# Optimization experiments

Measured on AMD Instinct MI355X. Metric: run time of the kernel, lower is better.

## Reference

```python
import jax, jax.numpy as jnp
import numpy as np

# dims (match init_kwargs / input_specs)
B, T, D = 64, 512, 128
H = 256          # hidden_size
W = 32           # cell_size
N = 64           # n_slots
R = 4            # n_reads
L = 2            # ctl_n_layers
TAU = 0.3
CLIP = 20.0
RW = R * W                      # read_size = 128
CTL_IN = D + RW                 # 256
CTL_OUT = 2 * RW + W + W        # 2*read + write cell + erase = 320
EPS = 1e-8


def setup_inputs() -> dict:
    key = jax.random.key(0)
    ks = jax.random.split(key, 10)
    s = lambda k, shape: jax.random.normal(k, shape, jnp.float32) * 0.05
    return {
        "x": jax.random.normal(ks[0], (B, T, D), jnp.float32),
        "h0": jax.random.normal(ks[1], (L, B, H), jnp.float32) * 0.1,
        # GRU layer 0 (PyTorch layout: [3H, in])
        "W_ih0": s(ks[2], (3 * H, CTL_IN)), "W_hh0": s(ks[3], (3 * H, H)),
        "b_ih0": jnp.zeros((3 * H,), jnp.float32), "b_hh0": jnp.zeros((3 * H,), jnp.float32),
        # GRU layer 1
        "W_ih1": s(ks[4], (3 * H, H)), "W_hh1": s(ks[5], (3 * H, H)),
        "b_ih1": jnp.zeros((3 * H,), jnp.float32), "b_hh1": jnp.zeros((3 * H,), jnp.float32),
        # interface Linear(H -> CTL_OUT) + ReLU
        "W_int": s(ks[6], (CTL_OUT, H)), "b_int": jnp.zeros((CTL_OUT,), jnp.float32),
        # mix gate Linear(2W -> W)
        "W_mix": s(ks[7], (W, 2 * W)), "b_mix": jnp.zeros((W,), jnp.float32),
    }


def _gru(xt, h, Wih, Whh, bih, bhh):
    gi = xt @ Wih.T + bih
    gh = h @ Whh.T + bhh
    ir, iz, inn = jnp.split(gi, 3, axis=-1)
    hr, hz, hn = jnp.split(gh, 3, axis=-1)
    r = jax.nn.sigmoid(ir + hr)
    z = jax.nn.sigmoid(iz + hz)
    n = jnp.tanh(inn + r * hn)
    return (1.0 - z) * n + z * h


def _cos_read(k, M, tau):
    # k: [b,R,W] keys, M: [b,N,W] memory -> content-based softmax read
    kn = k / (jnp.linalg.norm(k, axis=-1, keepdims=True) + EPS)
    Mn = M / (jnp.linalg.norm(M, axis=-1, keepdims=True) + EPS)
    w = jax.nn.softmax(jnp.einsum('brw,bnw->brn', kn, Mn) / tau, axis=-1)
    return jnp.einsum('brn,bnw->brw', w, M), w


def _forward(x, h0, W_ih0, W_hh0, b_ih0, b_hh0, W_ih1, W_hh1, b_ih1, b_hh1,
             W_int, b_int, W_mix, b_mix):
    bs = x.shape[0]

    def step(carry, inp):
        h0c, h1c, em, bm, l_read = carry
        xt, t = inp
        ctl = jnp.concatenate([xt, l_read], axis=-1)
        h0n = _gru(ctl, h0c, W_ih0, W_hh0, b_ih0, b_hh0)
        h1n = _gru(h0n, h1c, W_ih1, W_hh1, b_ih1, b_hh1)
        itf = jnp.clip(jax.nn.relu(h1n @ W_int.T + b_int), -CLIP, CLIP)
        k_em = itf[:, :RW].reshape(bs, R, W)
        k_bm = itf[:, RW:2 * RW].reshape(bs, R, W)
        m_t = itf[:, 2 * RW:2 * RW + W]          # write vector
        e_t = itf[:, 2 * RW + W:]                # erase vector
        # explicit memory: round-robin slot write (slot = t mod N), erase old content
        oh = jax.nn.one_hot(t % N, N, dtype=em.dtype)            # [N]
        em_erased = jnp.einsum('n,bnw->bw', oh, em)              # evicted slot
        em_new = em * (1.0 - oh)[None, :, None] + oh[None, :, None] * m_t[:, None, :]
        em_read, _ = _cos_read(k_em, em_new, TAU)
        # blurred memory: content read, then erase/accumulate evicted explicit slot
        bm_read, wb = _cos_read(k_bm, bm, 1.0)
        ww = wb.mean(axis=1)                                     # [b,N] write weights
        e = jax.nn.sigmoid(e_t)                                  # [b,W] bounded erase
        bm_new = bm * (1.0 - ww[:, :, None] * e[:, None, :]) \
                 + ww[:, :, None] * em_erased[:, None, :]
        # mix gate between explicit and blurred reads (per read head)
        g = jax.nn.sigmoid(jnp.concatenate([em_read, bm_read], -1) @ W_mix.T + b_mix)
        read = g * em_read + (1.0 - g) * bm_read                 # [b,R,W]
        l_new = read.reshape(bs, RW)
        out_t = jnp.concatenate([h0n, h1n, l_new], axis=-1)      # [b, 2H+RW]
        return (h0n, h1n, em_new, bm_new, l_new), out_t

    em0 = jnp.zeros((bs, N, W), x.dtype)
    bm0 = jnp.zeros((bs, N, W), x.dtype)
    lr0 = jnp.zeros((bs, RW), x.dtype)
    carry0 = (h0[0], h0[1], em0, bm0, lr0)
    xs = (jnp.swapaxes(x, 0, 1), jnp.arange(x.shape[1]))
    _, outs = jax.lax.scan(step, carry0, xs)                     # [T,b,2H+RW]
    return jnp.swapaxes(outs, 0, 1)                              # [b,T,2H+RW]


def reference(x, h0, W_ih0, W_hh0, b_ih0, b_hh0, W_ih1, W_hh1, b_ih1, b_hh1,
              W_int, b_int, W_mix, b_mix):
    return _forward(x, h0, W_ih0, W_hh0, b_ih0, b_hh0, W_ih1, W_hh1, b_ih1,
                    b_hh1, W_int, b_int, W_mix, b_mix)
```

## Files before the change

kernel.cpp:

```cpp
#include <hip/hip_runtime.h>
#include <hip/hip_bf16.h>
#include <stdint.h>

typedef unsigned int uint;
typedef unsigned short ushort;

#define TPB 768

#define OFF_A0 0
#define OFF_A1 (768*256)
#define OFF_A2 (2*768*256)
#define OFF_A3 (3*768*256)
#define OFF_A4 (4*768*256)
#define WS_USHORTS (4*768*256 + 320*256)

__device__ __forceinline__ float bflo(uint u){ return __uint_as_float(u << 16); }
__device__ __forceinline__ float bfhi(uint u){ return __uint_as_float(u & 0xffff0000u); }
__device__ __forceinline__ float sigm(float x){ return 1.0f / (1.0f + __expf(-x)); }
__device__ __forceinline__ float tanh_(float x){
    float xc = fminf(fmaxf(x, -15.0f), 15.0f);
    float e  = __expf(2.0f * xc);
    return (e - 1.0f) / (e + 1.0f);
}

__global__ void prep_kernel(const float* __restrict__ Wih0, const float* __restrict__ Whh0,
                            const float* __restrict__ Wih1, const float* __restrict__ Whh1,
                            const float* __restrict__ Wint, ushort* __restrict__ ws)
{
    int idx = blockIdx.x * 256 + threadIdx.x;
    if (idx >= WS_USHORTS) return;
    const float* src; int rows; int base; int p;
    if (idx < 4*768*256) {
        int m = idx / (768*256); p = idx % (768*256);
        src  = (m==0) ? Wih0 : (m==1) ? Whh0 : (m==2) ? Wih1 : Whh1;
        rows = 768; base = m * (768*256);
    } else {
        p = idx - 4*768*256; src = Wint; rows = 320; base = 4*768*256;
    }
    int kb  = p / (rows*8);
    int rem = p - kb*(rows*8);
    int j   = rem >> 3;
    int kl  = rem & 7;
    int k   = kb*8 + kl;
    __hip_bfloat16 h = __float2bfloat16(src[j*256 + k]);
    ws[base + p] = *reinterpret_cast<ushort*>(&h);
}

__device__ __forceinline__ void dual_mv(const ushort* __restrict__ Wi, const ushort* __restrict__ Wh,
                                        const float* vin, const float* hin,
                                        const float* __restrict__ bi, const float* __restrict__ bh,
                                        float* go_i, float* go_h, int tid)
{
    int j = tid;
    float ai = bi[j], ah = bh[j];
    const uint4* Pi = (const uint4*)Wi;
    const uint4* Ph = (const uint4*)Wh;
#pragma unroll 4
    for (int kb = 0; kb < 32; ++kb) {
        uint4 wi = Pi[kb*768 + j];
        uint4 wh = Ph[kb*768 + j];
        float4 va = *(const float4*)&vin[kb*8];
        float4 vb = *(const float4*)&vin[kb*8 + 4];
        float4 ha = *(const float4*)&hin[kb*8];
        float4 hb = *(const float4*)&hin[kb*8 + 4];
        ai += bflo(wi.x)*va.x + bfhi(wi.x)*va.y + bflo(wi.y)*va.z + bfhi(wi.y)*va.w
            + bflo(wi.z)*vb.x + bfhi(wi.z)*vb.y + bflo(wi.w)*vb.z + bfhi(wi.w)*vb.w;
        ah += bflo(wh.x)*ha.x + bfhi(wh.x)*ha.y + bflo(wh.y)*ha.z + bfhi(wh.y)*ha.w
            + bflo(wh.z)*hb.x + bfhi(wh.z)*hb.y + bflo(wh.w)*hb.z + bfhi(wh.w)*hb.w;
    }
    go_i[j] = ai; go_h[j] = ah;
}

__global__ __launch_bounds__(TPB) void ebm_main(
    const float* __restrict__ x, const float* __restrict__ h0i,
    const float* __restrict__ b_ih0, const float* __restrict__ b_hh0,
    const float* __restrict__ b_ih1, const float* __restrict__ b_hh1,
    const float* __restrict__ b_int, const float* __restrict__ Wmix,
    const float* __restrict__ bmix,
    const ushort* __restrict__ ws, float* __restrict__ out)
{
    __shared__ float v[256];
    __shared__ float gi[768], gh[768];
    __shared__ float h0s[256], h1s[256];
    __shared__ float lread[128];
    __shared__ float em[64][33], bm[64][33];
    __shared__ float itf[320];
    __shared__ float minv_em[64], minv_bm[64], kinv[8];
    __shared__ float sc[8][64];
    __shared__ float wwv[64], ev[32], emer[32];
    __shared__ float emrd[4][32], bmrd[4][32];
    __shared__ float wmix_s[32][65];

    const int tid = threadIdx.x;
    const int b   = blockIdx.x;

    if (tid < 256) { h0s[tid] = h0i[b*256 + tid]; h1s[tid] = h0i[(64 + b)*256 + tid]; }
    for (int i = tid; i < 64*33; i += TPB) { (&em[0][0])[i] = 0.f; (&bm[0][0])[i] = 0.f; }
    if (tid < 128) lread[tid] = 0.f;
    for (int i = tid; i < 32*64; i += TPB) { wmix_s[i >> 6][i & 63] = Wmix[i]; }
    __syncthreads();

    for (int t = 0; t < 512; ++t) {
        const size_t outbase = ((size_t)b*512 + t) * 640;

        if (tid < 128)      v[tid] = x[((size_t)b*512 + t)*128 + tid];
        else if (tid < 256) v[tid] = lread[tid - 128];
        __syncthreads();

        dual_mv(ws + OFF_A0, ws + OFF_A1, v, h0s, b_ih0, b_hh0, gi, gh, tid);
        __syncthreads();
        if (tid < 256) {
            float r  = sigm(gi[tid]       + gh[tid]);
            float z  = sigm(gi[256 + tid] + gh[256 + tid]);
            float n  = tanh_(gi[512 + tid] + r * gh[512 + tid]);
            float hn = (1.f - z) * n + z * h0s[tid];
            h0s[tid] = hn;
            out[outbase + tid] = hn;
        }
        __syncthreads();

        dual_mv(ws + OFF_A2, ws + OFF_A3, h0s, h1s, b_ih1, b_hh1, gi, gh, tid);
        __syncthreads();
        if (tid < 256) {
            float r  = sigm(gi[tid]       + gh[tid]);
            float z  = sigm(gi[256 + tid] + gh[256 + tid]);
            float n  = tanh_(gi[512 + tid] + r * gh[512 + tid]);
            float hn = (1.f - z) * n + z * h1s[tid];
            h1s[tid] = hn;
            out[outbase + 256 + tid] = hn;
        }
        __syncthreads();

        if (tid < 320) {
            float a = b_int[tid];
            const uint4* Pv = (const uint4*)(ws + OFF_A4);
#pragma unroll 4
            for (int kb = 0; kb < 32; ++kb) {
                uint4 wv = Pv[kb*320 + tid];
                float4 va = *(const float4*)&h1s[kb*8];
                float4 vb = *(const float4*)&h1s[kb*8 + 4];
                a += bflo(wv.x)*va.x + bfhi(wv.x)*va.y + bflo(wv.y)*va.z + bfhi(wv.y)*va.w
                   + bflo(wv.z)*vb.x + bfhi(wv.z)*vb.y + bflo(wv.w)*vb.z + bfhi(wv.w)*vb.w;
            }
            itf[tid] = fminf(fmaxf(a, 0.f), 20.f);
        }
        __syncthreads();

        const int slot = t & 63;
        if (tid < 32) {
            emer[tid] = em[slot][tid];
            em[slot][tid] = itf[256 + tid];
            ev[tid] = sigm(itf[288 + tid]);
        }
        if (tid >= 32 && tid < 40) {
            int r = tid - 32;
            const float* kk = &itf[r*32];
            float s = 0.f;
#pragma unroll
            for (int w2 = 0; w2 < 32; ++w2) { float q = kk[w2]; s += q*q; }
            kinv[r] = 1.f / (sqrtf(s) + 1e-8f);
        }
        __syncthreads();

        if (tid < 64) {
            float s = 0.f;
#pragma unroll
            for (int w2 = 0; w2 < 32; ++w2) { float q = em[tid][w2]; s += q*q; }
            minv_em[tid] = 1.f / (sqrtf(s) + 1e-8f);
        } else if (tid < 128) {
            int n = tid - 64; float s = 0.f;
#pragma unroll
            for (int w2 = 0; w2 < 32; ++w2) { float q = bm[n][w2]; s += q*q; }
            minv_bm[n] = 1.f / (sqrtf(s) + 1e-8f);
        }
        __syncthreads();

        if (tid < 512) {
            int mm = tid >> 8, r = (tid >> 6) & 3, n = tid & 63;
            const float* kk = &itf[mm*128 + r*32];
            const float (*M)[33] = mm ? bm : em;
            float d = 0.f;
#pragma unroll
            for (int w2 = 0; w2 < 32; ++w2) d += kk[w2] * M[n][w2];
            float val = d * kinv[mm*4 + r] * (mm ? minv_bm[n] : minv_em[n]);
            if (!mm) val /= 0.3f;
            sc[mm*4 + r][n] = val;
        }
        __syncthreads();

        {
            int wave = tid >> 6, lane = tid & 63;
            if (wave < 8) {
                float val = sc[wave][lane];
                float m = val;
                for (int o = 32; o > 0; o >>= 1) m = fmaxf(m, __shfl_xor(m, o));
                float e = __expf(val - m);
                float s = e;
                for (int o = 32; o > 0; o >>= 1) s += __shfl_xor(s, o);
                sc[wave][lane] = e / s;
            }
        }
        __syncthreads();

        if (tid < 64) wwv[tid] = 0.25f * (sc[4][tid] + sc[5][tid] + sc[6][tid] + sc[7][tid]);
        if (tid < 256) {
            int mm = tid >> 7, r = (tid >> 5) & 3, w2 = tid & 31;
            const float (*M)[33] = mm ? bm : em;
            const float* wr = sc[mm*4 + r];
            float a = 0.f;
#pragma unroll 8
            for (int n = 0; n < 64; ++n) a += wr[n] * M[n][w2];
            if (mm) bmrd[r][w2] = a; else emrd[r][w2] = a;
        }
        __syncthreads();

        if (tid < 128) {
            int r = tid >> 5, w2 = tid & 31;
            float a = bmix[w2];
#pragma unroll
            for (int c = 0; c < 32; ++c) a += wmix_s[w2][c]      * emrd[r][c];
#pragma unroll
            for (int c = 0; c < 32; ++c) a += wmix_s[w2][32 + c] * bmrd[r][c];
            float g  = sigm(a);
            float rd = g * emrd[r][w2] + (1.f - g) * bmrd[r][w2];
            lread[tid] = rd;
            out[outbase + 512 + tid] = rd;
        } else {
            for (int i2 = tid - 128; i2 < 2048; i2 += TPB - 128) {
                int n = i2 >> 5, w2 = i2 & 31;
                bm[n][w2] = bm[n][w2] * (1.f - wwv[n]*ev[w2]) + wwv[n]*emer[w2];
            }
        }
        __syncthreads();
    }
}

extern "C" void kernel_launch(void* const* d_in, const int* in_sizes, int n_in,
                              void* d_out, int out_size, void* d_ws, size_t ws_size,
                              hipStream_t stream)
{
    const float* x    = (const float*)d_in[0];
    const float* h0   = (const float*)d_in[1];
    const float* Wih0 = (const float*)d_in[2];
    const float* Whh0 = (const float*)d_in[3];
    const float* bih0 = (const float*)d_in[4];
    const float* bhh0 = (const float*)d_in[5];
    const float* Wih1 = (const float*)d_in[6];
    const float* Whh1 = (const float*)d_in[7];
    const float* bih1 = (const float*)d_in[8];
    const float* bhh1 = (const float*)d_in[9];
    const float* Wint = (const float*)d_in[10];
    const float* bint = (const float*)d_in[11];
    const float* Wmix = (const float*)d_in[12];
    const float* bmix = (const float*)d_in[13];
    ushort* ws = (ushort*)d_ws;
    float*  out = (float*)d_out;

    if (ws_size < (size_t)WS_USHORTS * sizeof(ushort)) return;

    prep_kernel<<<(WS_USHORTS + 255)/256, 256, 0, stream>>>(Wih0, Whh0, Wih1, Whh1, Wint, ws);
    ebm_main<<<64, TPB, 0, stream>>>(x, h0, bih0, bhh0, bih1, bhh1, bint, Wmix, bmix, ws, out);
}
```

Before: 12.03 ms.

## Split each batch's GRU across four cooperating blocks with global-flag syncs

Each batch row is now handled by four 256-thread blocks instead of one 768-thread block. Each block computes a quarter of the GRU gate rows and shares the new hidden states with the others through a global buffer, using release fences and spin-waits on per-step flags. The memory-read part is computed redundantly in all four blocks. The goal is to use more CUs and cut the per-block weight streaming on the serial recurrence, in exchange for two cross-block handshakes per timestep and repeated memory work. It also relies on all 256 blocks being resident at once, or the spin-waits deadlock.

```diff
diff --git a/kernel.cpp b/kernel.cpp
--- a/kernel.cpp
+++ b/kernel.cpp
@@ -5,7 +5,7 @@
 typedef unsigned int uint;
 typedef unsigned short ushort;
 
-#define TPB 768
+#define TPB 256
 
 #define OFF_A0 0
 #define OFF_A1 (768*256)
@@ -13,6 +13,9 @@
 #define OFF_A3 (3*768*256)
 #define OFF_A4 (4*768*256)
 #define WS_USHORTS (4*768*256 + 320*256)
+#define WB_BYTES ((size_t)WS_USHORTS * 2)
+#define HX_FLOATS (2*2*64*256)
+#define FL_UINTS (2*64*4)
 
 __device__ __forceinline__ float bflo(uint u){ return __uint_as_float(u << 16); }
 __device__ __forceinline__ float bfhi(uint u){ return __uint_as_float(u & 0xffff0000u); }
@@ -25,9 +28,11 @@
 
 __global__ void prep_kernel(const float* __restrict__ Wih0, const float* __restrict__ Whh0,
                             const float* __restrict__ Wih1, const float* __restrict__ Whh1,
-                            const float* __restrict__ Wint, ushort* __restrict__ ws)
+                            const float* __restrict__ Wint, ushort* __restrict__ ws,
+                            uint* __restrict__ fl)
 {
     int idx = blockIdx.x * 256 + threadIdx.x;
+    if (idx < FL_UINTS) fl[idx] = 0u;
     if (idx >= WS_USHORTS) return;
     const float* src; int rows; int base; int p;
     if (idx < 4*768*256) {
@@ -46,15 +51,30 @@
     ws[base + p] = *reinterpret_cast<ushort*>(&h);
 }
 
-__device__ __forceinline__ void dual_mv(const ushort* __restrict__ Wi, const ushort* __restrict__ Wh,
-                                        const float* vin, const float* hin,
-                                        const float* __restrict__ bi, const float* __restrict__ bh,
-                                        float* go_i, float* go_h, int tid)
-{
-    int j = tid;
-    float ai = bi[j], ah = bh[j];
+template<int ROWS>
+__device__ __forceinline__ float mv_row(const ushort* __restrict__ W, const float* vin,
+                                        float acc, int j)
+{
+    const uint4* P = (const uint4*)W;
+    float a0 = acc, a1 = 0.f;
+#pragma unroll 4
+    for (int kb = 0; kb < 32; ++kb) {
+        uint4 w = P[kb*ROWS + j];
+        float4 va = *(const float4*)&vin[kb*8];
+        float4 vb = *(const float4*)&vin[kb*8 + 4];
+        a0 += bflo(w.x)*va.x + bfhi(w.x)*va.y + bflo(w.y)*va.z + bfhi(w.y)*va.w;
+        a1 += bflo(w.z)*vb.x + bfhi(w.z)*vb.y + bflo(w.w)*vb.z + bfhi(w.w)*vb.w;
+    }
+    return a0 + a1;
+}
+
+__device__ __forceinline__ void dual_mv2(const ushort* __restrict__ Wi, const ushort* __restrict__ Wh,
+                                         const float* vin, const float* hin,
+                                         float bi, float bh, float* oi, float* oh, int j)
+{
     const uint4* Pi = (const uint4*)Wi;
     const uint4* Ph = (const uint4*)Wh;
+    float ai = bi, ah = bh;
 #pragma unroll 4
     for (int kb = 0; kb < 32; ++kb) {
         uint4 wi = Pi[kb*768 + j];
@@ -68,7 +88,17 @@
         ah += bflo(wh.x)*ha.x + bfhi(wh.x)*ha.y + bflo(wh.y)*ha.z + bfhi(wh.y)*ha.w
             + bflo(wh.z)*hb.x + bfhi(wh.z)*hb.y + bflo(wh.w)*hb.z + bfhi(wh.w)*hb.w;
     }
-    go_i[j] = ai; go_h[j] = ah;
+    *oi = ai; *oh = ah;
+}
+
+__device__ __forceinline__ void spin_ge(uint* f, uint v){
+    while (__hip_atomic_load(f, __ATOMIC_RELAXED, __HIP_MEMORY_SCOPE_AGENT) < v) {}
+}
+__device__ __forceinline__ float coh_ld(float* p){
+    return __hip_atomic_load(p, __ATOMIC_RELAXED, __HIP_MEMORY_SCOPE_AGENT);
+}
+__device__ __forceinline__ void coh_st(float* p, float v){
+    __hip_atomic_store(p, v, __ATOMIC_RELAXED, __HIP_MEMORY_SCOPE_AGENT);
 }
 
 __global__ __launch_bounds__(TPB) void ebm_main(
@@ -77,10 +107,11 @@
     const float* __restrict__ b_ih1, const float* __restrict__ b_hh1,
     const float* __restrict__ b_int, const float* __restrict__ Wmix,
     const float* __restrict__ bmix,
-    const ushort* __restrict__ ws, float* __restrict__ out)
+    const ushort* __restrict__ ws, float* __restrict__ hx, uint* __restrict__ fl,
+    float* __restrict__ out)
 {
     __shared__ float v[256];
-    __shared__ float gi[768], gh[768];
+    __shared__ float gi[192], gh[192];
     __shared__ float h0s[256], h1s[256];
     __shared__ float lread[128];
     __shared__ float em[64][33], bm[64][33];
@@ -92,57 +123,94 @@
     __shared__ float wmix_s[32][65];
 
     const int tid = threadIdx.x;
-    const int b   = blockIdx.x;
-
-    if (tid < 256) { h0s[tid] = h0i[b*256 + tid]; h1s[tid] = h0i[(64 + b)*256 + tid]; }
+    const int b   = blockIdx.x & 63;
+    const int q   = blockIdx.x >> 6;
+
+    h0s[tid] = h0i[b*256 + tid];
+    h1s[tid] = h0i[(64 + b)*256 + tid];
     for (int i = tid; i < 64*33; i += TPB) { (&em[0][0])[i] = 0.f; (&bm[0][0])[i] = 0.f; }
     if (tid < 128) lread[tid] = 0.f;
-    for (int i = tid; i < 32*64; i += TPB) { wmix_s[i >> 6][i & 63] = Wmix[i]; }
+    for (int i = tid; i < 32*64; i += TPB) wmix_s[i >> 6][i & 63] = Wmix[i];
     __syncthreads();
 
     for (int t = 0; t < 512; ++t) {
         const size_t outbase = ((size_t)b*512 + t) * 640;
-
-        if (tid < 128)      v[tid] = x[((size_t)b*512 + t)*128 + tid];
-        else if (tid < 256) v[tid] = lread[tid - 128];
-        __syncthreads();
-
-        dual_mv(ws + OFF_A0, ws + OFF_A1, v, h0s, b_ih0, b_hh0, gi, gh, tid);
-        __syncthreads();
-        if (tid < 256) {
+        const int par = t & 1;
+        const uint tv = (uint)(t + 1);
+
+        if (tid < 128) v[tid] = x[((size_t)b*512 + t)*128 + tid];
+        else           v[tid] = lread[tid - 128];
+        __syncthreads();
+
+        if (tid < 192) {
+            int g = tid >> 6, i = tid & 63;
+            int j = g*256 + q*64 + i;
+            dual_mv2(ws + OFF_A0, ws + OFF_A1, v, h0s, b_ih0[j], b_hh0[j], &gi[tid], &gh[tid], j);
+        }
+        __syncthreads();
+        if (tid < 64) {
             float r  = sigm(gi[tid]       + gh[tid]);
-            float z  = sigm(gi[256 + tid] + gh[256 + tid]);
-            float n  = tanh_(gi[512 + tid] + r * gh[512 + tid]);
-            float hn = (1.f - z) * n + z * h0s[tid];
-            h0s[tid] = hn;
-            out[outbase + tid] = hn;
-        }
-        __syncthreads();
-
-        dual_mv(ws + OFF_A2, ws + OFF_A3, h0s, h1s, b_ih1, b_hh1, gi, gh, tid);
-        __syncthreads();
-        if (tid < 256) {
+            float z  = sigm(gi[64 + tid]  + gh[64 + tid]);
+            float n  = tanh_(gi[128 + tid] + r * gh[128 + tid]);
+            float hn = (1.f - z) * n + z * h0s[q*64 + tid];
+            coh_st(&hx[((par*2 + 0)*64 + b)*256 + q*64 + tid], hn);
+            out[outbase + q*64 + tid] = hn;
+        }
+        __syncthreads();
+        if (tid == 0) {
+            __builtin_amdgcn_fence(__ATOMIC_RELEASE, "agent");
+            __hip_atomic_store(&fl[(0*64 + b)*4 + q], tv, __ATOMIC_RELAXED, __HIP_MEMORY_SCOPE_AGENT);
+        }
+
+        if (tid < 192) {
+            int g = tid >> 6, i = tid & 63;
+            int j = g*256 + q*64 + i;
+            gh[tid] = mv_row<768>(ws + OFF_A3, h1s, b_hh1[j], j);
+        } else {
+            int n = tid - 192; float s = 0.f;
+#pragma unroll
+            for (int w2 = 0; w2 < 32; ++w2) { float q2 = bm[n][w2]; s += q2*q2; }
+            minv_bm[n] = 1.f / (sqrtf(s) + 1e-8f);
+        }
+
+        if (tid < 4) spin_ge(&fl[(0*64 + b)*4 + tid], tv);
+        __syncthreads();
+        asm volatile("" ::: "memory");
+        h0s[tid] = coh_ld(&hx[((par*2 + 0)*64 + b)*256 + tid]);
+        __syncthreads();
+
+        if (tid < 192) {
+            int g = tid >> 6, i = tid & 63;
+            int j = g*256 + q*64 + i;
+            gi[tid] = mv_row<768>(ws + OFF_A2, h0s, b_ih1[j], j);
+        }
+        __syncthreads();
+        if (tid < 64) {
             float r  = sigm(gi[tid]       + gh[tid]);
-            float z  = sigm(gi[256 + tid] + gh[256 + tid]);
-            float n  = tanh_(gi[512 + tid] + r * gh[512 + tid]);
-            float hn = (1.f - z) * n + z * h1s[tid];
-            h1s[tid] = hn;
-            out[outbase + 256 + tid] = hn;
-        }
-        __syncthreads();
-
-        if (tid < 320) {
-            float a = b_int[tid];
-            const uint4* Pv = (const uint4*)(ws + OFF_A4);
-#pragma unroll 4
-            for (int kb = 0; kb < 32; ++kb) {
-                uint4 wv = Pv[kb*320 + tid];
-                float4 va = *(const float4*)&h1s[kb*8];
-                float4 vb = *(const float4*)&h1s[kb*8 + 4];
-                a += bflo(wv.x)*va.x + bfhi(wv.x)*va.y + bflo(wv.y)*va.z + bfhi(wv.y)*va.w
-                   + bflo(wv.z)*vb.x + bfhi(wv.z)*vb.y + bflo(wv.w)*vb.z + bfhi(wv.w)*vb.w;
+            float z  = sigm(gi[64 + tid]  + gh[64 + tid]);
+            float n  = tanh_(gi[128 + tid] + r * gh[128 + tid]);
+            float hn = (1.f - z) * n + z * h1s[q*64 + tid];
+            coh_st(&hx[((par*2 + 1)*64 + b)*256 + q*64 + tid], hn);
+            out[outbase + 256 + q*64 + tid] = hn;
+        }
+        __syncthreads();
+        if (tid == 0) {
+            __builtin_amdgcn_fence(__ATOMIC_RELEASE, "agent");
+            __hip_atomic_store(&fl[(1*64 + b)*4 + q], tv, __ATOMIC_RELAXED, __HIP_MEMORY_SCOPE_AGENT);
+        }
+        if (tid < 4) spin_ge(&fl[(1*64 + b)*4 + tid], tv);
+        __syncthreads();
+        asm volatile("" ::: "memory");
+        h1s[tid] = coh_ld(&hx[((par*2 + 1)*64 + b)*256 + tid]);
+        __syncthreads();
+
+        {
+            float a = mv_row<320>(ws + OFF_A4, h1s, b_int[tid], tid);
+            itf[tid] = fminf(fmaxf(a, 0.f), 20.f);
+            if (tid < 64) {
+                float a2 = mv_row<320>(ws + OFF_A4, h1s, b_int[256 + tid], 256 + tid);
+                itf[256 + tid] = fminf(fmaxf(a2, 0.f), 20.f);
             }
-            itf[tid] = fminf(fmaxf(a, 0.f), 20.f);
         }
         __syncthreads();
 
@@ -151,59 +219,52 @@
             emer[tid] = em[slot][tid];
             em[slot][tid] = itf[256 + tid];
             ev[tid] = sigm(itf[288 + tid]);
-        }
-        if (tid >= 32 && tid < 40) {
+        } else if (tid < 40) {
             int r = tid - 32;
             const float* kk = &itf[r*32];
             float s = 0.f;
 #pragma unroll
-            for (int w2 = 0; w2 < 32; ++w2) { float q = kk[w2]; s += q*q; }
+            for (int w2 = 0; w2 < 32; ++w2) { float q2 = kk[w2]; s += q2*q2; }
             kinv[r] = 1.f / (sqrtf(s) + 1e-8f);
         }
         __syncthreads();
-
         if (tid < 64) {
             float s = 0.f;
 #pragma unroll
-            for (int w2 = 0; w2 < 32; ++w2) { float q = em[tid][w2]; s += q*q; }
+            for (int w2 = 0; w2 < 32; ++w2) { float q2 = em[tid][w2]; s += q2*q2; }
             minv_em[tid] = 1.f / (sqrtf(s) + 1e-8f);
-        } else if (tid < 128) {
-            int n = tid - 64; float s = 0.f;
-#pragma unroll
-            for (int w2 = 0; w2 < 32; ++w2) { float q = bm[n][w2]; s += q*q; }
-            minv_bm[n] = 1.f / (sqrtf(s) + 1e-8f);
-        }
-        __syncthreads();
-
-        if (tid < 512) {
-            int mm = tid >> 8, r = (tid >> 6) & 3, n = tid & 63;
+        }
+        __syncthreads();
+#pragma unroll
+        for (int it = 0; it < 2; ++it) {
+            int idx = tid + it*256;
+            int mm = idx >> 8, r = (idx >> 6) & 3, n = idx & 63;
             const float* kk = &itf[mm*128 + r*32];
             const float (*M)[33] = mm ? bm : em;
             float d = 0.f;
 #pragma unroll
             for (int w2 = 0; w2 < 32; ++w2) d += kk[w2] * M[n][w2];
             float val = d * kinv[mm*4 + r] * (mm ? minv_bm[n] : minv_em[n]);
-            if (!mm) val /= 0.3f;
+            if (!mm) val *= (1.f/0.3f);
             sc[mm*4 + r][n] = val;
         }
         __syncthreads();
-
         {
             int wave = tid >> 6, lane = tid & 63;
-            if (wave < 8) {
-                float val = sc[wave][lane];
+#pragma unroll
+            for (int rr = wave; rr < 8; rr += 4) {
+                float val = sc[rr][lane];
                 float m = val;
                 for (int o = 32; o > 0; o >>= 1) m = fmaxf(m, __shfl_xor(m, o));
                 float e = __expf(val - m);
                 float s = e;
                 for (int o = 32; o > 0; o >>= 1) s += __shfl_xor(s, o);
-                sc[wave][lane] = e / s;
+                sc[rr][lane] = e / s;
             }
         }
         __syncthreads();
-
         if (tid < 64) wwv[tid] = 0.25f * (sc[4][tid] + sc[5][tid] + sc[6][tid] + sc[7][tid]);
-        if (tid < 256) {
+        {
             int mm = tid >> 7, r = (tid >> 5) & 3, w2 = tid & 31;
             const float (*M)[33] = mm ? bm : em;
             const float* wr = sc[mm*4 + r];
@@ -213,7 +274,6 @@
             if (mm) bmrd[r][w2] = a; else emrd[r][w2] = a;
         }
         __syncthreads();
-
         if (tid < 128) {
             int r = tid >> 5, w2 = tid & 31;
             float a = bmix[w2];
@@ -224,7 +284,7 @@
             float g  = sigm(a);
             float rd = g * emrd[r][w2] + (1.f - g) * bmrd[r][w2];
             lread[tid] = rd;
-            out[outbase + 512 + tid] = rd;
+            if (q == 0) out[outbase + 512 + tid] = rd;
         } else {
             for (int i2 = tid - 128; i2 < 2048; i2 += TPB - 128) {
                 int n = i2 >> 5, w2 = i2 & 31;
@@ -253,11 +313,16 @@
     const float* bint = (const float*)d_in[11];
     const float* Wmix = (const float*)d_in[12];
     const float* bmix = (const float*)d_in[13];
+
     ushort* ws = (ushort*)d_ws;
+    float*  hx = (float*)((char*)d_ws + WB_BYTES);
+    uint*   fl = (uint*)((char*)d_ws + WB_BYTES + (size_t)HX_FLOATS*4);
     float*  out = (float*)d_out;
 
-    if (ws_size < (size_t)WS_USHORTS * sizeof(ushort)) return;
-
-    prep_kernel<<<(WS_USHORTS + 255)/256, 256, 0, stream>>>(Wih0, Whh0, Wih1, Whh1, Wint, ws);
-    ebm_main<<<64, TPB, 0, stream>>>(x, h0, bih0, bhh0, bih1, bhh1, bint, Wmix, bmix, ws, out);
-}
+    const size_t need = WB_BYTES + (size_t)HX_FLOATS*4 + (size_t)FL_UINTS*4;
+    if (ws_size < need) return;
+
+    prep_kernel<<<(WS_USHORTS + 255)/256, 256, 0, stream>>>(Wih0, Whh0, Wih1, Whh1, Wint, ws, fl);
+    ebm_main<<<256, TPB, 0, stream>>>(x, h0, bih0, bhh0, bih1, bhh1, bint, Wmix, bmix,
+                                      ws, hx, fl, out);
+}
```

New measurement: 18.04 ms. 50.0% more time.

## Switch weights to fp16 and split GRU matvecs so each thread handles one matrix

Applied to the files above, without the earlier changes.

Weights are now stored as fp16 instead of bf16. The matvecs are restructured so threads 0-383 compute two rows of the input-gate matrix and threads 384-767 compute two rows of the hidden matrix, instead of every thread doing one row of both. The interface matvec uses 160 threads with two rows each, and each row uses two partial accumulators to shorten the dependency chain. The work per thread is the same, but each thread now streams from only one matrix, and fp16 changes the weight rounding compared with bf16.

```diff
diff --git a/kernel.cpp b/kernel.cpp
--- a/kernel.cpp
+++ b/kernel.cpp
@@ -1,5 +1,6 @@
 #include <hip/hip_runtime.h>
 #include <hip/hip_bf16.h>
+#include <hip/hip_fp16.h>
 #include <stdint.h>
 
 typedef unsigned int uint;
@@ -14,8 +15,9 @@
 #define OFF_A4 (4*768*256)
 #define WS_USHORTS (4*768*256 + 320*256)
 
-__device__ __forceinline__ float bflo(uint u){ return __uint_as_float(u << 16); }
-__device__ __forceinline__ float bfhi(uint u){ return __uint_as_float(u & 0xffff0000u); }
+__device__ __forceinline__ __half2 h2cast(uint u){
+    union { uint u; __half2 h; } c; c.u = u; return c.h;
+}
 __device__ __forceinline__ float sigm(float x){ return 1.0f / (1.0f + __expf(-x)); }
 __device__ __forceinline__ float tanh_(float x){
     float xc = fminf(fmaxf(x, -15.0f), 15.0f);
@@ -42,33 +44,35 @@
     int j   = rem >> 3;
     int kl  = rem & 7;
     int k   = kb*8 + kl;
-    __hip_bfloat16 h = __float2bfloat16(src[j*256 + k]);
+    __half h = __float2half_rn(src[j*256 + k]);
     ws[base + p] = *reinterpret_cast<ushort*>(&h);
 }
 
-__device__ __forceinline__ void dual_mv(const ushort* __restrict__ Wi, const ushort* __restrict__ Wh,
-                                        const float* vin, const float* hin,
-                                        const float* __restrict__ bi, const float* __restrict__ bh,
-                                        float* go_i, float* go_h, int tid)
-{
-    int j = tid;
-    float ai = bi[j], ah = bh[j];
-    const uint4* Pi = (const uint4*)Wi;
-    const uint4* Ph = (const uint4*)Wh;
+template<int ROWS>
+__device__ __forceinline__ void mv2_row(const ushort* __restrict__ W, const float* vin,
+                                        float b0, float b1, float* o0, float* o1,
+                                        int j0, int j1)
+{
+    const uint4* P = (const uint4*)W;
+    float p0a = b0, p0b = 0.f, p1a = b1, p1b = 0.f;
 #pragma unroll 4
     for (int kb = 0; kb < 32; ++kb) {
-        uint4 wi = Pi[kb*768 + j];
-        uint4 wh = Ph[kb*768 + j];
+        uint4 w0 = P[kb*ROWS + j0];
+        uint4 w1 = P[kb*ROWS + j1];
         float4 va = *(const float4*)&vin[kb*8];
         float4 vb = *(const float4*)&vin[kb*8 + 4];
-        float4 ha = *(const float4*)&hin[kb*8];
-        float4 hb = *(const float4*)&hin[kb*8 + 4];
-        ai += bflo(wi.x)*va.x + bfhi(wi.x)*va.y + bflo(wi.y)*va.z + bfhi(wi.y)*va.w
-            + bflo(wi.z)*vb.x + bfhi(wi.z)*vb.y + bflo(wi.w)*vb.z + bfhi(wi.w)*vb.w;
-        ah += bflo(wh.x)*ha.x + bfhi(wh.x)*ha.y + bflo(wh.y)*ha.z + bfhi(wh.y)*ha.w
-            + bflo(wh.z)*hb.x + bfhi(wh.z)*hb.y + bflo(wh.w)*hb.z + bfhi(wh.w)*hb.w;
+        __half2 h;
+        h = h2cast(w0.x); p0a += __low2float(h)*va.x; p0a += __high2float(h)*va.y;
+        h = h2cast(w0.y); p0a += __low2float(h)*va.z; p0a += __high2float(h)*va.w;
+        h = h2cast(w0.z); p0b += __low2float(h)*vb.x; p0b += __high2float(h)*vb.y;
+        h = h2cast(w0.w); p0b += __low2float(h)*vb.z; p0b += __high2float(h)*vb.w;
+        h = h2cast(w1.x); p1a += __low2float(h)*va.x; p1a += __high2float(h)*va.y;
+        h = h2cast(w1.y); p1a += __low2float(h)*va.z; p1a += __high2float(h)*va.w;
+        h = h2cast(w1.z); p1b += __low2float(h)*vb.x; p1b += __high2float(h)*vb.y;
+        h = h2cast(w1.w); p1b += __low2float(h)*vb.z; p1b += __high2float(h)*vb.w;
     }
-    go_i[j] = ai; go_h[j] = ah;
+    *o0 = p0a + p0b;
+    *o1 = p1a + p1b;
 }
 
 __global__ __launch_bounds__(TPB) void ebm_main(
@@ -107,7 +111,14 @@
         else if (tid < 256) v[tid] = lread[tid - 128];
         __syncthreads();
 
-        dual_mv(ws + OFF_A0, ws + OFF_A1, v, h0s, b_ih0, b_hh0, gi, gh, tid);
+        if (tid < 384) {
+            mv2_row<768>(ws + OFF_A0, v, b_ih0[tid], b_ih0[tid + 384],
+                         &gi[tid], &gi[tid + 384], tid, tid + 384);
+        } else {
+            int i = tid - 384;
+            mv2_row<768>(ws + OFF_A1, h0s, b_hh0[i], b_hh0[i + 384],
+                         &gh[i], &gh[i + 384], i, i + 384);
+        }
         __syncthreads();
         if (tid < 256) {
             float r  = sigm(gi[tid]       + gh[tid]);
@@ -119,7 +130,14 @@
         }
         __syncthreads();
 
-        dual_mv(ws + OFF_A2, ws + OFF_A3, h0s, h1s, b_ih1, b_hh1, gi, gh, tid);
+        if (tid < 384) {
+            mv2_row<768>(ws + OFF_A2, h0s, b_ih1[tid], b_ih1[tid + 384],
+                         &gi[tid], &gi[tid + 384], tid, tid + 384);
+        } else {
+            int i = tid - 384;
+            mv2_row<768>(ws + OFF_A3, h1s, b_hh1[i], b_hh1[i + 384],
+                         &gh[i], &gh[i + 384], i, i + 384);
+        }
         __syncthreads();
         if (tid < 256) {
             float r  = sigm(gi[tid]       + gh[tid]);
@@ -131,18 +149,12 @@
         }
         __syncthreads();
 
-        if (tid < 320) {
-            float a = b_int[tid];
-            const uint4* Pv = (const uint4*)(ws + OFF_A4);
-#pragma unroll 4
-            for (int kb = 0; kb < 32; ++kb) {
-                uint4 wv = Pv[kb*320 + tid];
-                float4 va = *(const float4*)&h1s[kb*8];
-                float4 vb = *(const float4*)&h1s[kb*8 + 4];
-                a += bflo(wv.x)*va.x + bfhi(wv.x)*va.y + bflo(wv.y)*va.z + bfhi(wv.y)*va.w
-                   + bflo(wv.z)*vb.x + bfhi(wv.z)*vb.y + bflo(wv.w)*vb.z + bfhi(wv.w)*vb.w;
-            }
-            itf[tid] = fminf(fmaxf(a, 0.f), 20.f);
+        if (tid < 160) {
+            float a0, a1;
+            mv2_row<320>(ws + OFF_A4, h1s, b_int[tid], b_int[tid + 160],
+                         &a0, &a1, tid, tid + 160);
+            itf[tid]       = fminf(fmaxf(a0, 0.f), 20.f);
+            itf[tid + 160] = fminf(fmaxf(a1, 0.f), 20.f);
         }
         __syncthreads();
 
@@ -183,7 +195,7 @@
 #pragma unroll
             for (int w2 = 0; w2 < 32; ++w2) d += kk[w2] * M[n][w2];
             float val = d * kinv[mm*4 + r] * (mm ? minv_bm[n] : minv_em[n]);
-            if (!mm) val /= 0.3f;
+            if (!mm) val *= (1.f/0.3f);
             sc[mm*4 + r][n] = val;
         }
         __syncthreads();
```

Result: slower. 12.47 ms (+3.7%).

## Merge per-step phases to cut barriers, prefetch next x, switch weights to fp16

Applied to the files above, without the earlier changes.

Restructures the per-timestep schedule to remove several __syncthreads barriers. The score, softmax and read phases are fused into one wave-level phase, with key norms computed inline and the freshly written slot read directly from itf. The next timestep's x row is loaded during the final phase, and the em slot write is deferred, so neither needs its own barrier. The weight cache changes from bf16 to fp16 with split accumulators, which changes rounding and could overflow if weights were large; each thread now also recomputes the key norms redundantly.

```diff
diff --git a/kernel.cpp b/kernel.cpp
--- a/kernel.cpp
+++ b/kernel.cpp
@@ -1,5 +1,5 @@
 #include <hip/hip_runtime.h>
-#include <hip/hip_bf16.h>
+#include <hip/hip_fp16.h>
 #include <stdint.h>
 
 typedef unsigned int uint;
@@ -14,8 +14,9 @@
 #define OFF_A4 (4*768*256)
 #define WS_USHORTS (4*768*256 + 320*256)
 
-__device__ __forceinline__ float bflo(uint u){ return __uint_as_float(u << 16); }
-__device__ __forceinline__ float bfhi(uint u){ return __uint_as_float(u & 0xffff0000u); }
+__device__ __forceinline__ __half2 h2cast(uint u){
+    union { uint u; __half2 h; } c; c.u = u; return c.h;
+}
 __device__ __forceinline__ float sigm(float x){ return 1.0f / (1.0f + __expf(-x)); }
 __device__ __forceinline__ float tanh_(float x){
     float xc = fminf(fmaxf(x, -15.0f), 15.0f);
@@ -42,19 +43,17 @@
     int j   = rem >> 3;
     int kl  = rem & 7;
     int k   = kb*8 + kl;
-    __hip_bfloat16 h = __float2bfloat16(src[j*256 + k]);
+    __half h = __float2half_rn(src[j*256 + k]);
     ws[base + p] = *reinterpret_cast<ushort*>(&h);
 }
 
 __device__ __forceinline__ void dual_mv(const ushort* __restrict__ Wi, const ushort* __restrict__ Wh,
                                         const float* vin, const float* hin,
-                                        const float* __restrict__ bi, const float* __restrict__ bh,
-                                        float* go_i, float* go_h, int tid)
-{
-    int j = tid;
-    float ai = bi[j], ah = bh[j];
+                                        float bi, float bh, float* oi, float* oh, int j)
+{
     const uint4* Pi = (const uint4*)Wi;
     const uint4* Ph = (const uint4*)Wh;
+    float ai = bi, a2 = 0.f, ah = bh, b2 = 0.f;
 #pragma unroll 4
     for (int kb = 0; kb < 32; ++kb) {
         uint4 wi = Pi[kb*768 + j];
@@ -63,12 +62,36 @@
         float4 vb = *(const float4*)&vin[kb*8 + 4];
         float4 ha = *(const float4*)&hin[kb*8];
         float4 hb = *(const float4*)&hin[kb*8 + 4];
-        ai += bflo(wi.x)*va.x + bfhi(wi.x)*va.y + bflo(wi.y)*va.z + bfhi(wi.y)*va.w
-            + bflo(wi.z)*vb.x + bfhi(wi.z)*vb.y + bflo(wi.w)*vb.z + bfhi(wi.w)*vb.w;
-        ah += bflo(wh.x)*ha.x + bfhi(wh.x)*ha.y + bflo(wh.y)*ha.z + bfhi(wh.y)*ha.w
-            + bflo(wh.z)*hb.x + bfhi(wh.z)*hb.y + bflo(wh.w)*hb.z + bfhi(wh.w)*hb.w;
-    }
-    go_i[j] = ai; go_h[j] = ah;
+        __half2 h;
+        h = h2cast(wi.x); ai += __low2float(h)*va.x; ai += __high2float(h)*va.y;
+        h = h2cast(wi.y); ai += __low2float(h)*va.z; ai += __high2float(h)*va.w;
+        h = h2cast(wi.z); a2 += __low2float(h)*vb.x; a2 += __high2float(h)*vb.y;
+        h = h2cast(wi.w); a2 += __low2float(h)*vb.z; a2 += __high2float(h)*vb.w;
+        h = h2cast(wh.x); ah += __low2float(h)*ha.x; ah += __high2float(h)*ha.y;
+        h = h2cast(wh.y); ah += __low2float(h)*ha.z; ah += __high2float(h)*ha.w;
+        h = h2cast(wh.z); b2 += __low2float(h)*hb.x; b2 += __high2float(h)*hb.y;
+        h = h2cast(wh.w); b2 += __low2float(h)*hb.z; b2 += __high2float(h)*hb.w;
+    }
+    *oi = ai + a2; *oh = ah + b2;
+}
+
+__device__ __forceinline__ float mv1(const ushort* __restrict__ W, const float* vin,
+                                     float b0, int j)
+{
+    const uint4* P = (const uint4*)W;
+    float p0 = b0, q0 = 0.f;
+#pragma unroll 4
+    for (int kb = 0; kb < 32; ++kb) {
+        uint4 w = P[kb*320 + j];
+        float4 va = *(const float4*)&vin[kb*8];
+        float4 vb = *(const float4*)&vin[kb*8 + 4];
+        __half2 h;
+        h = h2cast(w.x); p0 += __low2float(h)*va.x; p0 += __high2float(h)*va.y;
+        h = h2cast(w.y); p0 += __low2float(h)*va.z; p0 += __high2float(h)*va.w;
+        h = h2cast(w.z); q0 += __low2float(h)*vb.x; q0 += __high2float(h)*vb.y;
+        h = h2cast(w.w); q0 += __low2float(h)*vb.z; q0 += __high2float(h)*vb.w;
+    }
+    return p0 + q0;
 }
 
 __global__ __launch_bounds__(TPB) void ebm_main(
@@ -82,12 +105,11 @@
     __shared__ float v[256];
     __shared__ float gi[768], gh[768];
     __shared__ float h0s[256], h1s[256];
-    __shared__ float lread[128];
     __shared__ float em[64][33], bm[64][33];
     __shared__ float itf[320];
-    __shared__ float minv_em[64], minv_bm[64], kinv[8];
+    __shared__ float minv_em[64], minv_bm[64];
     __shared__ float sc[8][64];
-    __shared__ float wwv[64], ev[32], emer[32];
+    __shared__ float ev[32], emer[32];
     __shared__ float emrd[4][32], bmrd[4][32];
     __shared__ float wmix_s[32][65];
 
@@ -96,19 +118,18 @@
 
     if (tid < 256) { h0s[tid] = h0i[b*256 + tid]; h1s[tid] = h0i[(64 + b)*256 + tid]; }
     for (int i = tid; i < 64*33; i += TPB) { (&em[0][0])[i] = 0.f; (&bm[0][0])[i] = 0.f; }
-    if (tid < 128) lread[tid] = 0.f;
-    for (int i = tid; i < 32*64; i += TPB) { wmix_s[i >> 6][i & 63] = Wmix[i]; }
+    if (tid < 128)      v[128 + tid] = 0.f;
+    else if (tid < 256) v[tid - 128] = x[((size_t)b*512)*128 + (tid - 128)];
+    for (int i = tid; i < 32*64; i += TPB) wmix_s[i >> 6][i & 63] = Wmix[i];
     __syncthreads();
 
     for (int t = 0; t < 512; ++t) {
         const size_t outbase = ((size_t)b*512 + t) * 640;
-
-        if (tid < 128)      v[tid] = x[((size_t)b*512 + t)*128 + tid];
-        else if (tid < 256) v[tid] = lread[tid - 128];
-        __syncthreads();
-
-        dual_mv(ws + OFF_A0, ws + OFF_A1, v, h0s, b_ih0, b_hh0, gi, gh, tid);
-        __syncthreads();
+        const int slot = t & 63;
+
+        dual_mv(ws + OFF_A0, ws + OFF_A1, v, h0s, b_ih0[tid], b_hh0[tid], &gi[tid], &gh[tid], tid);
+        __syncthreads();
+
         if (tid < 256) {
             float r  = sigm(gi[tid]       + gh[tid]);
             float z  = sigm(gi[256 + tid] + gh[256 + tid]);
@@ -119,8 +140,9 @@
         }
         __syncthreads();
 
-        dual_mv(ws + OFF_A2, ws + OFF_A3, h0s, h1s, b_ih1, b_hh1, gi, gh, tid);
-        __syncthreads();
+        dual_mv(ws + OFF_A2, ws + OFF_A3, h0s, h1s, b_ih1[tid], b_hh1[tid], &gi[tid], &gh[tid], tid);
+        __syncthreads();
+
         if (tid < 256) {
             float r  = sigm(gi[tid]       + gh[tid]);
             float z  = sigm(gi[256 + tid] + gh[256 + tid]);
@@ -132,43 +154,15 @@
         __syncthreads();
 
         if (tid < 320) {
-            float a = b_int[tid];
-            const uint4* Pv = (const uint4*)(ws + OFF_A4);
-#pragma unroll 4
-            for (int kb = 0; kb < 32; ++kb) {
-                uint4 wv = Pv[kb*320 + tid];
-                float4 va = *(const float4*)&h1s[kb*8];
-                float4 vb = *(const float4*)&h1s[kb*8 + 4];
-                a += bflo(wv.x)*va.x + bfhi(wv.x)*va.y + bflo(wv.y)*va.z + bfhi(wv.y)*va.w
-                   + bflo(wv.z)*vb.x + bfhi(wv.z)*vb.y + bflo(wv.w)*vb.z + bfhi(wv.w)*vb.w;
-            }
+            float a = mv1(ws + OFF_A4, h1s, b_int[tid], tid);
             itf[tid] = fminf(fmaxf(a, 0.f), 20.f);
-        }
-        __syncthreads();
-
-        const int slot = t & 63;
-        if (tid < 32) {
-            emer[tid] = em[slot][tid];
-            em[slot][tid] = itf[256 + tid];
-            ev[tid] = sigm(itf[288 + tid]);
-        }
-        if (tid >= 32 && tid < 40) {
-            int r = tid - 32;
-            const float* kk = &itf[r*32];
-            float s = 0.f;
-#pragma unroll
-            for (int w2 = 0; w2 < 32; ++w2) { float q = kk[w2]; s += q*q; }
-            kinv[r] = 1.f / (sqrtf(s) + 1e-8f);
-        }
-        __syncthreads();
-
-        if (tid < 64) {
-            float s = 0.f;
-#pragma unroll
-            for (int w2 = 0; w2 < 32; ++w2) { float q = em[tid][w2]; s += q*q; }
-            minv_em[tid] = 1.f / (sqrtf(s) + 1e-8f);
-        } else if (tid < 128) {
-            int n = tid - 64; float s = 0.f;
+        } else if (tid < 384) {
+            int n = tid - 320; float s = 0.f;
+#pragma unroll
+            for (int w2 = 0; w2 < 32; ++w2) { float q = em[n][w2]; s += q*q; }
+            minv_em[n] = 1.f / (sqrtf(s) + 1e-8f);
+        } else if (tid < 448) {
+            int n = tid - 384; float s = 0.f;
 #pragma unroll
             for (int w2 = 0; w2 < 32; ++w2) { float q = bm[n][w2]; s += q*q; }
             minv_bm[n] = 1.f / (sqrtf(s) + 1e-8f);
@@ -176,41 +170,50 @@
         __syncthreads();
 
         if (tid < 512) {
-            int mm = tid >> 8, r = (tid >> 6) & 3, n = tid & 63;
-            const float* kk = &itf[mm*128 + r*32];
-            const float (*M)[33] = mm ? bm : em;
-            float d = 0.f;
-#pragma unroll
-            for (int w2 = 0; w2 < 32; ++w2) d += kk[w2] * M[n][w2];
-            float val = d * kinv[mm*4 + r] * (mm ? minv_bm[n] : minv_em[n]);
-            if (!mm) val /= 0.3f;
-            sc[mm*4 + r][n] = val;
-        }
-        __syncthreads();
-
-        {
-            int wave = tid >> 6, lane = tid & 63;
-            if (wave < 8) {
-                float val = sc[wave][lane];
-                float m = val;
-                for (int o = 32; o > 0; o >>= 1) m = fmaxf(m, __shfl_xor(m, o));
-                float e = __expf(val - m);
-                float s = e;
-                for (int o = 32; o > 0; o >>= 1) s += __shfl_xor(s, o);
-                sc[wave][lane] = e / s;
+            const int row = tid >> 6;
+            const int mm  = row >> 2;
+            const int n   = tid & 63;
+            const float* kk = &itf[mm*128 + (row & 3)*32];
+            float ks = 0.f;
+#pragma unroll
+            for (int w2 = 0; w2 < 32; ++w2) ks += kk[w2]*kk[w2];
+            const float kinv = 1.f / (sqrtf(ks) + 1e-8f);
+            float d, minv;
+            if (mm == 0 && n == slot) {
+                float dd = 0.f, ss = 0.f;
+#pragma unroll
+                for (int w2 = 0; w2 < 32; ++w2) { float m_ = itf[256 + w2]; dd += kk[w2]*m_; ss += m_*m_; }
+                d = dd; minv = 1.f / (sqrtf(ss) + 1e-8f);
+            } else {
+                const float (*M)[33] = mm ? bm : em;
+                float dd = 0.f;
+#pragma unroll
+                for (int w2 = 0; w2 < 32; ++w2) dd += kk[w2] * M[n][w2];
+                d = dd; minv = mm ? minv_bm[n] : minv_em[n];
             }
-        }
-        __syncthreads();
-
-        if (tid < 64) wwv[tid] = 0.25f * (sc[4][tid] + sc[5][tid] + sc[6][tid] + sc[7][tid]);
-        if (tid < 256) {
-            int mm = tid >> 7, r = (tid >> 5) & 3, w2 = tid & 31;
-            const float (*M)[33] = mm ? bm : em;
-            const float* wr = sc[mm*4 + r];
-            float a = 0.f;
+            float val = d * kinv * minv;
+            if (!mm) val *= (1.f/0.3f);
+            float m = val;
+            for (int o = 32; o > 0; o >>= 1) m = fmaxf(m, __shfl_xor(m, o));
+            float e = __expf(val - m);
+            float s = e;
+            for (int o = 32; o > 0; o >>= 1) s += __shfl_xor(s, o);
+            sc[row][n] = e / s;
+            if (n < 32) {
+                const int w2 = n;
+                float a = 0.f;
 #pragma unroll 8
-            for (int n = 0; n < 64; ++n) a += wr[n] * M[n][w2];
-            if (mm) bmrd[r][w2] = a; else emrd[r][w2] = a;
+                for (int nn = 0; nn < 64; ++nn) {
+                    float m_ = mm ? bm[nn][w2]
+                                  : ((nn == slot) ? itf[256 + w2] : em[nn][w2]);
+                    a += sc[row][nn] * m_;
+                }
+                if (mm) bmrd[row & 3][w2] = a; else emrd[row & 3][w2] = a;
+            }
+        } else if (tid < 544) {
+            emer[tid - 512] = em[slot][tid - 512];
+        } else if (tid < 576) {
+            ev[tid - 544] = sigm(itf[288 + (tid - 544)]);
         }
         __syncthreads();
 
@@ -223,12 +226,18 @@
             for (int c = 0; c < 32; ++c) a += wmix_s[w2][32 + c] * bmrd[r][c];
             float g  = sigm(a);
             float rd = g * emrd[r][w2] + (1.f - g) * bmrd[r][w2];
-            lread[tid] = rd;
+            v[128 + tid] = rd;
             out[outbase + 512 + tid] = rd;
+        } else if (tid < 160) {
+            em[slot][tid - 128] = itf[256 + (tid - 128)];
+        } else if (tid < 288) {
+            int k = tid - 160;
+            if (t + 1 < 512) v[k] = x[((size_t)b*512 + t + 1)*128 + k];
         } else {
-            for (int i2 = tid - 128; i2 < 2048; i2 += TPB - 128) {
+            for (int i2 = tid - 288; i2 < 2048; i2 += TPB - 288) {
                 int n = i2 >> 5, w2 = i2 & 31;
-                bm[n][w2] = bm[n][w2] * (1.f - wwv[n]*ev[w2]) + wwv[n]*emer[w2];
+                float ww = 0.25f * (sc[4][n] + sc[5][n] + sc[6][n] + sc[7][n]);
+                bm[n][w2] = bm[n][w2] * (1.f - ww*ev[w2]) + ww*emer[w2];
             }
         }
         __syncthreads();
@@ -253,7 +262,7 @@
     const float* bint = (const float*)d_in[11];
     const float* Wmix = (const float*)d_in[12];
     const float* bmix = (const float*)d_in[13];
-    ushort* ws = (ushort*)d_ws;
+    ushort* ws  = (ushort*)d_ws;
     float*  out = (float*)d_out;
 
     if (ws_size < (size_t)WS_USHORTS * sizeof(ushort)) return;
```

After: 12.54 ms. +4.3%, slower.
